# Performance work log

Measured on AMD Instinct MI355X. Metric: run time of the kernel, lower is better.

Reference implementation:

```python
import jax, jax.numpy as jnp
import numpy as np

NUM_LSTMS = 2
INPUT_DIM = 1
HIDDEN_DIM = 32
OUTPUT_DIM = 1


def _init_cell(key, in_dim, hid):
    k1, k2, k3, k4 = jax.random.split(key, 4)
    s = 1.0 / np.sqrt(hid)
    Wih = jax.random.uniform(k1, (4 * hid, in_dim), minval=-s, maxval=s, dtype=jnp.float32)
    Whh = jax.random.uniform(k2, (4 * hid, hid), minval=-s, maxval=s, dtype=jnp.float32)
    bih = jax.random.uniform(k3, (4 * hid,), minval=-s, maxval=s, dtype=jnp.float32)
    bhh = jax.random.uniform(k4, (4 * hid,), minval=-s, maxval=s, dtype=jnp.float32)
    # forget-gate bias (second quarter in PyTorch i,f,g,o layout) filled with 1.0
    bih = bih.at[hid:2 * hid].set(1.0)
    bhh = bhh.at[hid:2 * hid].set(1.0)
    return Wih, Whh, bih, bhh


def setup_inputs() -> dict:
    key = jax.random.key(0)
    kx, k0, k1, kl = jax.random.split(key, 4)
    B, T = 2048, 1024
    x = jax.random.normal(kx, (B, T), dtype=jnp.float32)
    Wih0, Whh0, bih0, bhh0 = _init_cell(k0, INPUT_DIM, HIDDEN_DIM)
    Wih1, Whh1, bih1, bhh1 = _init_cell(k1, HIDDEN_DIM, HIDDEN_DIM)
    kw, kb = jax.random.split(kl)
    s = 1.0 / np.sqrt(HIDDEN_DIM)
    Wlin = jax.random.uniform(kw, (OUTPUT_DIM, HIDDEN_DIM), minval=-s, maxval=s, dtype=jnp.float32)
    blin = jax.random.uniform(kb, (OUTPUT_DIM,), minval=-s, maxval=s, dtype=jnp.float32)
    return {"x": x, "Wih0": Wih0, "Whh0": Whh0, "bih0": bih0, "bhh0": bhh0,
            "Wih1": Wih1, "Whh1": Whh1, "bih1": bih1, "bhh1": bhh1,
            "Wlin": Wlin, "blin": blin}


def _lstm_cell(x_t, h, c, Wih, Whh, bih, bhh):
    # PyTorch LSTMCell gate layout: i, f, g, o
    g = x_t @ Wih.T + bih + h @ Whh.T + bhh  # [B, 4H]
    i, f, gg, o = jnp.split(g, 4, axis=-1)
    i = jax.nn.sigmoid(i)
    f = jax.nn.sigmoid(f)
    gg = jnp.tanh(gg)
    o = jax.nn.sigmoid(o)
    c_new = f * c + i * gg
    h_new = o * jnp.tanh(c_new)
    return h_new, c_new


def reference(x, Wih0, Whh0, bih0, bhh0, Wih1, Whh1, bih1, bhh1, Wlin, blin):
    B, T = x.shape
    params = [(Wih0, Whh0, bih0, bhh0), (Wih1, Whh1, bih1, bhh1)]
    h0 = [jnp.zeros((B, HIDDEN_DIM), jnp.float32) for _ in range(NUM_LSTMS)]
    c0 = [jnp.zeros((B, HIDDEN_DIM), jnp.float32) for _ in range(NUM_LSTMS)]

    xs = x.T[:, :, None]  # [T, B, 1]

    def step(carry, x_t):
        hs, cs = carry
        hs, cs = list(hs), list(cs)
        inp = x_t
        for j in range(NUM_LSTMS):
            hs[j], cs[j] = _lstm_cell(inp, hs[j], cs[j], *params[j])
            inp = hs[j]
        out = hs[-1] @ Wlin.T + blin  # [B, 1]
        return (tuple(hs), tuple(cs)), out

    _, outs = jax.lax.scan(step, (tuple(h0), tuple(c0)), xs)  # [T, B, 1]
    return outs[:, :, 0].T  # [B, T]
```

## Files before the change

kernel.cpp:

```cpp
#include <hip/hip_runtime.h>


typedef float f2 __attribute__((ext_vector_type(2)));
typedef float f4 __attribute__((ext_vector_type(4)));

constexpr int BATCH = 2048;
constexpr int TLEN  = 1024;
constexpr int HID   = 32;
constexpr float L2E = 1.44269504088896f;

union F4U { f4 v; f2 p[2]; };

static __device__ __forceinline__ float rcp_f(float v){ return __builtin_amdgcn_rcpf(v); }
static __device__ __forceinline__ float exp2_f(float v){ return __builtin_amdgcn_exp2f(v); }
static __device__ __forceinline__ float bcastf(float v, int k){
    return __int_as_float(__builtin_amdgcn_readlane(__float_as_int(v), k));
}
static __device__ __forceinline__ f2 fma2(f2 a, f2 b, f2 c){
    return __builtin_elementwise_fma(a, b, c);
}
static __device__ __forceinline__ float xchg32(float v, int xaddr){
    return __int_as_float(__builtin_amdgcn_ds_bpermute(xaddr, __float_as_int(v)));
}

__global__ void __launch_bounds__(256) __attribute__((amdgpu_waves_per_eu(2, 2)))
lstm2_v13(const float* __restrict__ x,
          const float* __restrict__ Wih0, const float* __restrict__ Whh0,
          const float* __restrict__ bih0, const float* __restrict__ bhh0,
          const float* __restrict__ Wih1, const float* __restrict__ Whh1,
          const float* __restrict__ bih1, const float* __restrict__ bhh1,
          const float* __restrict__ Wlin, const float* __restrict__ blin,
          float* __restrict__ out)
{
    const int tid  = threadIdx.x;
    const int lane = tid & 63;
    const int w    = tid >> 6;
    const int b    = blockIdx.x * 4 + w;
    const int j    = lane & 31;
    const int hi   = lane >> 5;
    const int rowA = hi * 64 + j;
    const int rowB = rowA + 32;
    const int xaddr = (lane ^ 32) << 2;

    __shared__ alignas(16) float hb0[4][32];
    __shared__ alignas(16) float hb1[4][32];
    __shared__ alignas(16) float hstore[4][64][36];
    __shared__ alignas(16) float wls[32];

    hb0[w][j] = 0.0f;
    hb1[w][j] = 0.0f;
    wls[j] = Wlin[j];

    f2 wA0[16], wB0[16], iA1[16], iB1[16], hA1[16], hB1[16];
    #pragma unroll
    for (int m = 0; m < 16; ++m){
        wA0[m] = *(const f2*)&Whh0[rowA * HID + 2*m];
        wB0[m] = *(const f2*)&Whh0[rowB * HID + 2*m];
        iA1[m] = *(const f2*)&Wih1[rowA * HID + 2*m];
        iB1[m] = *(const f2*)&Wih1[rowB * HID + 2*m];
        hA1[m] = *(const f2*)&Whh1[rowA * HID + 2*m];
        hB1[m] = *(const f2*)&Whh1[rowB * HID + 2*m];
    }
    const float wa0 = Wih0[rowA];
    const float wb0 = Wih0[rowB];
    const float ba0 = bih0[rowA] + bhh0[rowA];
    const float bb0 = bih0[rowB] + bhh0[rowB];
    const float ba1 = bih1[rowA] + bhh1[rowA];
    const float bb1 = bih1[rowB] + bhh1[rowB];
    const float bl  = blin[0];

    const float kA = hi ? (-2.0f * L2E) : (-L2E);
    const float mA = hi ?  2.0f : 1.0f;
    const float cA = hi ? -1.0f : 0.0f;

    float c0 = 0.0f, c1 = 0.0f;

    const float* xrow = x   + (size_t)b * TLEN;
    float*       orow = out + (size_t)b * TLEN;

    const f4* h0v = (const f4*)&hb0[w][0];
    const f4* h1v = (const f4*)&hb1[w][0];

    for (int tc = 0; tc < TLEN / 64; ++tc){
        const float xchunk = xrow[tc * 64 + lane];

        for (int tt = 0; tt < 64; ++tt){
            const float xt = bcastf(xchunk, tt);

            f2 aA  = {__builtin_fmaf(wa0, xt, ba0), 0.0f};
            f2 aB  = {__builtin_fmaf(wb0, xt, bb0), 0.0f};
            f2 aA2 = {0.0f, 0.0f}, aB2 = {0.0f, 0.0f};
            #pragma unroll
            for (int r = 0; r < 8; ++r){
                F4U hh; hh.v = h0v[r];
                aA  = fma2(wA0[2*r],   hh.p[0], aA );
                aB  = fma2(wB0[2*r],   hh.p[0], aB );
                aA2 = fma2(wA0[2*r+1], hh.p[1], aA2);
                aB2 = fma2(wB0[2*r+1], hh.p[1], aB2);
            }
            const float ga = (aA.x + aA2.x) + (aA.y + aA2.y);
            const float gb = (aB.x + aB2.x) + (aB.y + aB2.y);

            float act_a = __builtin_fmaf(mA, rcp_f(1.0f + exp2_f(ga * kA)), cA);
            float act_b = rcp_f(1.0f + exp2_f(gb * (-L2E)));
            const float oa = xchg32(act_a, xaddr);
            const float ob = xchg32(act_b, xaddr);
            {
                const float fsel = hi ? ob : act_b;
                const float osel = hi ? act_b : ob;
                c0 = __builtin_fmaf(fsel, c0, act_a * oa);
                const float t0 = __builtin_fmaf(2.0f,
                        rcp_f(1.0f + exp2_f(c0 * (-2.0f * L2E))), -1.0f);
                const float h0 = osel * t0;
                hb0[w][j] = h0;
            }

            f2 pA  = {ba1, 0.0f}, pB = {bb1, 0.0f};
            f2 pA2 = {0.0f, 0.0f}, pB2 = {0.0f, 0.0f};
            #pragma unroll
            for (int r = 0; r < 8; ++r){
                F4U hn; hn.v = h0v[r];
                F4U ho; ho.v = h1v[r];
                pA  = fma2(iA1[2*r],   hn.p[0], pA );
                pB  = fma2(iB1[2*r],   hn.p[0], pB );
                pA2 = fma2(iA1[2*r+1], hn.p[1], pA2);
                pB2 = fma2(iB1[2*r+1], hn.p[1], pB2);
                pA  = fma2(hA1[2*r],   ho.p[0], pA );
                pB  = fma2(hB1[2*r],   ho.p[0], pB );
                pA2 = fma2(hA1[2*r+1], ho.p[1], pA2);
                pB2 = fma2(hB1[2*r+1], ho.p[1], pB2);
            }
            const float g1a = (pA.x + pA2.x) + (pA.y + pA2.y);
            const float g1b = (pB.x + pB2.x) + (pB.y + pB2.y);

            float act_a1 = __builtin_fmaf(mA, rcp_f(1.0f + exp2_f(g1a * kA)), cA);
            float act_b1 = rcp_f(1.0f + exp2_f(g1b * (-L2E)));
            const float oa1 = xchg32(act_a1, xaddr);
            const float ob1 = xchg32(act_b1, xaddr);
            {
                const float fsel = hi ? ob1 : act_b1;
                const float osel = hi ? act_b1 : ob1;
                c1 = __builtin_fmaf(fsel, c1, act_a1 * oa1);
                const float t1 = __builtin_fmaf(2.0f,
                        rcp_f(1.0f + exp2_f(c1 * (-2.0f * L2E))), -1.0f);
                const float h1 = osel * t1;
                hb1[w][j] = h1;
                hstore[w][tt][j] = h1;
            }
        }

        {
            const f4* hv = (const f4*)&hstore[w][lane][0];
            const f4* wv = (const f4*)&wls[0];
            f2 y = {bl, 0.0f}, y2 = {0.0f, 0.0f};
            #pragma unroll
            for (int r = 0; r < 8; ++r){
                F4U hh; hh.v = hv[r];
                F4U ww; ww.v = wv[r];
                y  = fma2(ww.p[0], hh.p[0], y );
                y2 = fma2(ww.p[1], hh.p[1], y2);
            }
            orow[tc * 64 + lane] = (y.x + y2.x) + (y.y + y2.y);
        }
    }
}

extern "C" void kernel_launch(void* const* d_in, const int* in_sizes, int n_in,
                              void* d_out, int out_size, void* d_ws, size_t ws_size,
                              hipStream_t stream) {
    const float* x    = (const float*)d_in[0];
    const float* Wih0 = (const float*)d_in[1];
    const float* Whh0 = (const float*)d_in[2];
    const float* bih0 = (const float*)d_in[3];
    const float* bhh0 = (const float*)d_in[4];
    const float* Wih1 = (const float*)d_in[5];
    const float* Whh1 = (const float*)d_in[6];
    const float* bih1 = (const float*)d_in[7];
    const float* bhh1 = (const float*)d_in[8];
    const float* Wlin = (const float*)d_in[9];
    const float* blin = (const float*)d_in[10];
    float* outp = (float*)d_out;

    dim3 block(256);
    dim3 grid(BATCH / 4);
    hipLaunchKernelGGL(lstm2_v13, grid, block, 0, stream,
                       x, Wih0, Whh0, bih0, bhh0, Wih1, Whh1, bih1, bhh1,
                       Wlin, blin, outp);
}
```

Before: 869.1 us.

## Split each batch row across two waves with one gate row per lane

The kernel now uses one 128-thread block per batch element. Each lane owns a single gate row instead of two, so per-lane FMA work and weight registers are halved. Hidden states are shared through double-buffered LDS and a 64-entry ring for layer 1, and gate values are gathered with four ds_bpermute calls. The aim is a shorter serial dependency chain per step and more waves for hiding latency, at the cost of two block barriers per timestep and extra cross-lane traffic.

```diff
diff --git a/kernel.cpp b/kernel.cpp
--- a/kernel.cpp
+++ b/kernel.cpp
@@ -19,12 +19,12 @@
 static __device__ __forceinline__ f2 fma2(f2 a, f2 b, f2 c){
     return __builtin_elementwise_fma(a, b, c);
 }
-static __device__ __forceinline__ float xchg32(float v, int xaddr){
-    return __int_as_float(__builtin_amdgcn_ds_bpermute(xaddr, __float_as_int(v)));
+static __device__ __forceinline__ float bperm(int addr, float v){
+    return __int_as_float(__builtin_amdgcn_ds_bpermute(addr, __float_as_int(v)));
 }
 
-__global__ void __launch_bounds__(256) __attribute__((amdgpu_waves_per_eu(2, 2)))
-lstm2_v13(const float* __restrict__ x,
+__global__ void __launch_bounds__(128)
+lstm2_v14(const float* __restrict__ x,
           const float* __restrict__ Wih0, const float* __restrict__ Whh0,
           const float* __restrict__ bih0, const float* __restrict__ bhh0,
           const float* __restrict__ Wih1, const float* __restrict__ Whh1,
@@ -32,127 +32,120 @@
           const float* __restrict__ Wlin, const float* __restrict__ blin,
           float* __restrict__ out)
 {
-    const int tid  = threadIdx.x;
-    const int lane = tid & 63;
-    const int w    = tid >> 6;
-    const int b    = blockIdx.x * 4 + w;
-    const int j    = lane & 31;
-    const int hi   = lane >> 5;
-    const int rowA = hi * 64 + j;
-    const int rowB = rowA + 32;
-    const int xaddr = (lane ^ 32) << 2;
+    const int tid = threadIdx.x;
+    const int l   = tid & 63;
+    const int q   = tid >> 6;
+    const int b   = blockIdx.x;
+    const int g   = l >> 4;
+    const int u   = q * 16 + (l & 15);
+    const int R   = 32 * g + u;
 
-    __shared__ alignas(16) float hb0[4][32];
-    __shared__ alignas(16) float hb1[4][32];
-    __shared__ alignas(16) float hstore[4][64][36];
-    __shared__ alignas(16) float wls[32];
+    __shared__ alignas(16) float h0r[2][32];
+    __shared__ alignas(16) float h1s[64][36];
+    __shared__ alignas(16) float wlb[32];
 
-    hb0[w][j] = 0.0f;
-    hb1[w][j] = 0.0f;
-    wls[j] = Wlin[j];
+    if (g == 0){
+        h0r[0][u] = 0.0f; h0r[1][u] = 0.0f;
+        h1s[63][u] = 0.0f;
+        wlb[u] = Wlin[u];
+    }
 
-    f2 wA0[16], wB0[16], iA1[16], iB1[16], hA1[16], hB1[16];
+    f2 w0[16], wi[16], wh[16];
     #pragma unroll
     for (int m = 0; m < 16; ++m){
-        wA0[m] = *(const f2*)&Whh0[rowA * HID + 2*m];
-        wB0[m] = *(const f2*)&Whh0[rowB * HID + 2*m];
-        iA1[m] = *(const f2*)&Wih1[rowA * HID + 2*m];
-        iB1[m] = *(const f2*)&Wih1[rowB * HID + 2*m];
-        hA1[m] = *(const f2*)&Whh1[rowA * HID + 2*m];
-        hB1[m] = *(const f2*)&Whh1[rowB * HID + 2*m];
+        w0[m] = *(const f2*)&Whh0[R * HID + 2*m];
+        wi[m] = *(const f2*)&Wih1[R * HID + 2*m];
+        wh[m] = *(const f2*)&Whh1[R * HID + 2*m];
     }
-    const float wa0 = Wih0[rowA];
-    const float wb0 = Wih0[rowB];
-    const float ba0 = bih0[rowA] + bhh0[rowA];
-    const float bb0 = bih0[rowB] + bhh0[rowB];
-    const float ba1 = bih1[rowA] + bhh1[rowA];
-    const float bb1 = bih1[rowB] + bhh1[rowB];
-    const float bl  = blin[0];
+    const float wx = Wih0[R];
+    const float b0 = bih0[R] + bhh0[R];
+    const float b1 = bih1[R] + bhh1[R];
+    const float bl = blin[0];
 
-    const float kA = hi ? (-2.0f * L2E) : (-L2E);
-    const float mA = hi ?  2.0f : 1.0f;
-    const float cA = hi ? -1.0f : 0.0f;
+    const bool  isT = (g == 2);
+    const float kA = isT ? (-2.0f * L2E) : (-L2E);
+    const float mA = isT ?  2.0f : 1.0f;
+    const float cA = isT ? -1.0f : 0.0f;
+
+    const int a_i = (l & 15) << 2;
+    const int a_f = a_i + 64;
+    const int a_g = a_i + 128;
+    const int a_o = a_i + 192;
 
     float c0 = 0.0f, c1 = 0.0f;
 
     const float* xrow = x   + (size_t)b * TLEN;
     float*       orow = out + (size_t)b * TLEN;
 
-    const f4* h0v = (const f4*)&hb0[w][0];
-    const f4* h1v = (const f4*)&hb1[w][0];
+    __syncthreads();
 
     for (int tc = 0; tc < TLEN / 64; ++tc){
-        const float xchunk = xrow[tc * 64 + lane];
+        const float xchunk = xrow[tc * 64 + l];
 
         for (int tt = 0; tt < 64; ++tt){
             const float xt = bcastf(xchunk, tt);
 
-            f2 aA  = {__builtin_fmaf(wa0, xt, ba0), 0.0f};
-            f2 aB  = {__builtin_fmaf(wb0, xt, bb0), 0.0f};
-            f2 aA2 = {0.0f, 0.0f}, aB2 = {0.0f, 0.0f};
-            #pragma unroll
-            for (int r = 0; r < 8; ++r){
-                F4U hh; hh.v = h0v[r];
-                aA  = fma2(wA0[2*r],   hh.p[0], aA );
-                aB  = fma2(wB0[2*r],   hh.p[0], aB );
-                aA2 = fma2(wA0[2*r+1], hh.p[1], aA2);
-                aB2 = fma2(wB0[2*r+1], hh.p[1], aB2);
+            f2 aA  = {__builtin_fmaf(wx, xt, b0), 0.0f};
+            f2 aA2 = {0.0f, 0.0f};
+            {
+                const f4* hv = (const f4*)&h0r[(tt + 1) & 1][0];
+                #pragma unroll
+                for (int r = 0; r < 8; ++r){
+                    F4U hh; hh.v = hv[r];
+                    aA  = fma2(w0[2*r],   hh.p[0], aA );
+                    aA2 = fma2(w0[2*r+1], hh.p[1], aA2);
+                }
             }
-            const float ga = (aA.x + aA2.x) + (aA.y + aA2.y);
-            const float gb = (aB.x + aB2.x) + (aB.y + aB2.y);
+            const float g0v = (aA.x + aA.y) + (aA2.x + aA2.y);
+            const float av0 = __builtin_fmaf(mA, rcp_f(1.0f + exp2_f(g0v * kA)), cA);
+            const float iv0 = bperm(a_i, av0);
+            const float fv0 = bperm(a_f, av0);
+            const float gv0 = bperm(a_g, av0);
+            const float ov0 = bperm(a_o, av0);
+            c0 = __builtin_fmaf(fv0, c0, iv0 * gv0);
+            const float t0 = __builtin_fmaf(2.0f,
+                    rcp_f(1.0f + exp2_f(c0 * (-2.0f * L2E))), -1.0f);
+            const float h0n = ov0 * t0;
+            if (g == 0) h0r[tt & 1][u] = h0n;
+            __syncthreads();
 
-            float act_a = __builtin_fmaf(mA, rcp_f(1.0f + exp2_f(ga * kA)), cA);
-            float act_b = rcp_f(1.0f + exp2_f(gb * (-L2E)));
-            const float oa = xchg32(act_a, xaddr);
-            const float ob = xchg32(act_b, xaddr);
+            f2 pA  = {b1, 0.0f};
+            f2 pA2 = {0.0f, 0.0f};
             {
-                const float fsel = hi ? ob : act_b;
-                const float osel = hi ? act_b : ob;
-                c0 = __builtin_fmaf(fsel, c0, act_a * oa);
-                const float t0 = __builtin_fmaf(2.0f,
-                        rcp_f(1.0f + exp2_f(c0 * (-2.0f * L2E))), -1.0f);
-                const float h0 = osel * t0;
-                hb0[w][j] = h0;
+                const f4* hv = (const f4*)&h0r[tt & 1][0];
+                #pragma unroll
+                for (int r = 0; r < 8; ++r){
+                    F4U hh; hh.v = hv[r];
+                    pA  = fma2(wi[2*r],   hh.p[0], pA );
+                    pA2 = fma2(wi[2*r+1], hh.p[1], pA2);
+                }
+                const f4* hv1 = (const f4*)&h1s[(tt + 63) & 63][0];
+                #pragma unroll
+                for (int r = 0; r < 8; ++r){
+                    F4U hh; hh.v = hv1[r];
+                    pA  = fma2(wh[2*r],   hh.p[0], pA );
+                    pA2 = fma2(wh[2*r+1], hh.p[1], pA2);
+                }
             }
-
-            f2 pA  = {ba1, 0.0f}, pB = {bb1, 0.0f};
-            f2 pA2 = {0.0f, 0.0f}, pB2 = {0.0f, 0.0f};
-            #pragma unroll
-            for (int r = 0; r < 8; ++r){
-                F4U hn; hn.v = h0v[r];
-                F4U ho; ho.v = h1v[r];
-                pA  = fma2(iA1[2*r],   hn.p[0], pA );
-                pB  = fma2(iB1[2*r],   hn.p[0], pB );
-                pA2 = fma2(iA1[2*r+1], hn.p[1], pA2);
-                pB2 = fma2(iB1[2*r+1], hn.p[1], pB2);
-                pA  = fma2(hA1[2*r],   ho.p[0], pA );
-                pB  = fma2(hB1[2*r],   ho.p[0], pB );
-                pA2 = fma2(hA1[2*r+1], ho.p[1], pA2);
-                pB2 = fma2(hB1[2*r+1], ho.p[1], pB2);
-            }
-            const float g1a = (pA.x + pA2.x) + (pA.y + pA2.y);
-            const float g1b = (pB.x + pB2.x) + (pB.y + pB2.y);
-
-            float act_a1 = __builtin_fmaf(mA, rcp_f(1.0f + exp2_f(g1a * kA)), cA);
-            float act_b1 = rcp_f(1.0f + exp2_f(g1b * (-L2E)));
-            const float oa1 = xchg32(act_a1, xaddr);
-            const float ob1 = xchg32(act_b1, xaddr);
-            {
-                const float fsel = hi ? ob1 : act_b1;
-                const float osel = hi ? act_b1 : ob1;
-                c1 = __builtin_fmaf(fsel, c1, act_a1 * oa1);
-                const float t1 = __builtin_fmaf(2.0f,
-                        rcp_f(1.0f + exp2_f(c1 * (-2.0f * L2E))), -1.0f);
-                const float h1 = osel * t1;
-                hb1[w][j] = h1;
-                hstore[w][tt][j] = h1;
-            }
+            const float g1v = (pA.x + pA.y) + (pA2.x + pA2.y);
+            const float av1 = __builtin_fmaf(mA, rcp_f(1.0f + exp2_f(g1v * kA)), cA);
+            const float iv1 = bperm(a_i, av1);
+            const float fv1 = bperm(a_f, av1);
+            const float gv1 = bperm(a_g, av1);
+            const float ov1 = bperm(a_o, av1);
+            c1 = __builtin_fmaf(fv1, c1, iv1 * gv1);
+            const float t1 = __builtin_fmaf(2.0f,
+                    rcp_f(1.0f + exp2_f(c1 * (-2.0f * L2E))), -1.0f);
+            const float h1n = ov1 * t1;
+            if (g == 0) h1s[tt][u] = h1n;
+            __syncthreads();
         }
 
-        {
-            const f4* hv = (const f4*)&hstore[w][lane][0];
-            const f4* wv = (const f4*)&wls[0];
-            f2 y = {bl, 0.0f}, y2 = {0.0f, 0.0f};
+        if (q == 0){
+            const f4* hv = (const f4*)&h1s[l][0];
+            const f4* wv = (const f4*)&wlb[0];
+            f2 y  = {bl, 0.0f};
+            f2 y2 = {0.0f, 0.0f};
             #pragma unroll
             for (int r = 0; r < 8; ++r){
                 F4U hh; hh.v = hv[r];
@@ -160,7 +153,7 @@
                 y  = fma2(ww.p[0], hh.p[0], y );
                 y2 = fma2(ww.p[1], hh.p[1], y2);
             }
-            orow[tc * 64 + lane] = (y.x + y2.x) + (y.y + y2.y);
+            orow[tc * 64 + l] = (y.x + y.y) + (y2.x + y2.y);
         }
     }
 }
@@ -181,9 +174,9 @@
     const float* blin = (const float*)d_in[10];
     float* outp = (float*)d_out;
 
-    dim3 block(256);
-    dim3 grid(BATCH / 4);
-    hipLaunchKernelGGL(lstm2_v13, grid, block, 0, stream,
+    dim3 block(128);
+    dim3 grid(BATCH);
+    hipLaunchKernelGGL(lstm2_v14, grid, block, 0, stream,
                        x, Wih0, Whh0, bih0, bhh0, Wih1, Whh1, bih1, bhh1,
                        Wlin, blin, outp);
 }
```

Measured after the change: 1.583 ms. +82.1%, slower.
